# Optimization experiments

Measured on AMD Instinct MI355X. Metric: run time of the kernel, lower is better.

The kernel has to match this reference:

```python
import math
import jax, jax.numpy as jnp
import numpy as np

D_MODEL = 1024
N_HEADS = 16
HEAD_DIM = D_MODEL // N_HEADS
D_FF = 4096
LN_EPS = 1e-5


def _layer_norm(x, g, b):
    mu = jnp.mean(x, axis=-1, keepdims=True)
    var = jnp.var(x, axis=-1, keepdims=True)
    return (x - mu) * jax.lax.rsqrt(var + LN_EPS) * g + b


def setup_inputs() -> dict:
    key = jax.random.key(0)
    ks = jax.random.split(key, 8)
    s = 0.02
    d, dff = D_MODEL, D_FF
    return {
        "src": jax.random.normal(ks[0], (2, 2048, d), dtype=jnp.float32),
        "in_proj_w": jax.random.normal(ks[1], (3 * d, d), dtype=jnp.float32) * s,
        "in_proj_b": jnp.zeros((3 * d,), dtype=jnp.float32),
        "out_w": jax.random.normal(ks[2], (d, d), dtype=jnp.float32) * s,
        "out_b": jnp.zeros((d,), dtype=jnp.float32),
        "lin1_w": jax.random.normal(ks[3], (dff, d), dtype=jnp.float32) * s,
        "lin1_b": jnp.zeros((dff,), dtype=jnp.float32),
        "lin2_w": jax.random.normal(ks[4], (d, dff), dtype=jnp.float32) * s,
        "lin2_b": jnp.zeros((d,), dtype=jnp.float32),
        "ln1_g": jnp.ones((d,), dtype=jnp.float32),
        "ln1_b": jnp.zeros((d,), dtype=jnp.float32),
        "ln2_g": jnp.ones((d,), dtype=jnp.float32),
        "ln2_b": jnp.zeros((d,), dtype=jnp.float32),
    }


def reference(src, in_proj_w, in_proj_b, out_w, out_b, lin1_w, lin1_b,
              lin2_w, lin2_b, ln1_g, ln1_b, ln2_g, ln2_b):
    B, S, d = src.shape
    # QKV projections (in_proj_weight split at d, then kv split)
    q = src @ in_proj_w[:d].T + in_proj_b[:d]              # [B,S,d]
    kv = src @ in_proj_w[d:].T + in_proj_b[d:]             # [B,S,2d]
    q = q.reshape(B, S, N_HEADS, HEAD_DIM)
    kv = kv.reshape(B, S, 2, N_HEADS, HEAD_DIM)
    k, v = kv[:, :, 0], kv[:, :, 1]
    softmax_scale = 1.0 / math.sqrt(HEAD_DIM)
    scores = jnp.einsum('bthd,bshd->bhts', q, k) * softmax_scale  # [B,H,Sq,Skv]
    # 'distribute': softmax over the QUERY dimension (dim=-2)
    attention = jax.nn.softmax(scores, axis=-2)
    post = jnp.einsum('bhts,bshd->bthd', attention, v)     # [B,Sq,H,hd]
    # post-attention activation 'gelu' (torch exact gelu)
    post = jax.nn.gelu(post, approximate=False)
    # attention_scale == 'sqrt': divide by sqrt(kv_len)
    post = post / math.sqrt(S)
    attn_out = post.reshape(B, S, d) @ out_w.T + out_b
    # post-norm residual structure (pre_norm=False, dropout=0)
    x = _layer_norm(src + attn_out, ln1_g, ln1_b)
    ff = jax.nn.gelu(x @ lin1_w.T + lin1_b, approximate=False) @ lin2_w.T + lin2_b
    return _layer_norm(x + ff, ln2_g, ln2_b)
```

## Files before the change

### kernel.cpp

```cpp
#include <hip/hip_runtime.h>
#include <hip/hip_bf16.h>
#include <math.h>


using bf16x8 = __attribute__((ext_vector_type(8))) short;
using f32x4  = __attribute__((ext_vector_type(4))) float;

__device__ inline f32x4 mfma16(bf16x8 a, bf16x8 b, f32x4 c) {
    return __builtin_amdgcn_mfma_f32_16x16x32_bf16(a, b, c, 0, 0, 0);
}

__device__ inline ushort f2bf(float f) {
    union { float f; unsigned u; } x; x.f = f;
    unsigned r = x.u + 0x7fffu + ((x.u >> 16) & 1u);
    return (ushort)(r >> 16);
}

__device__ inline float bf2f(ushort u) {
    union { unsigned u; float f; } x; x.u = ((unsigned)u) << 16; return x.f;
}

__device__ inline unsigned pk2bf(float a, float b) {
    __hip_bfloat162 h = __float22bfloat162_rn(float2{a, b});
    union { __hip_bfloat162 h; unsigned u; } x; x.h = h;
    return x.u;
}

__device__ inline float gelu_fast(float v) {
    float u = v * (1.5957691216f + 0.0713548162f * v * v);
    float e = __expf(u);
    return v * (e / (e + 1.0f));
}

__device__ __forceinline__ void gl2lds16(const ushort* g, ushort* l) {
    __builtin_amdgcn_global_load_lds(
        (const __attribute__((address_space(1))) unsigned int*)g,
        (__attribute__((address_space(3))) unsigned int*)l,
        16, 0, 0);
}

__global__ __launch_bounds__(256) void cvt_all(const float4* __restrict__ s0,
                                               const float4* __restrict__ s1,
                                               const float4* __restrict__ s2,
                                               const float4* __restrict__ s3,
                                               const float4* __restrict__ s4,
                                               ushort4* __restrict__ out) {
    int i = blockIdx.x * 256 + threadIdx.x;
    const float4* p;
    int off;
    if (i < 1048576)      { p = s0; off = i; }
    else if (i < 1835008) { p = s1; off = i - 1048576; }
    else if (i < 2097152) { p = s2; off = i - 1835008; }
    else if (i < 3145728) { p = s3; off = i - 2097152; }
    else                  { p = s4; off = i - 3145728; }
    float4 v = p[off];
    ushort4 o;
    o.x = f2bf(v.x); o.y = f2bf(v.y); o.z = f2bf(v.z); o.w = f2bf(v.w);
    out[i] = o;
}

__global__ __launch_bounds__(256) void gemm_bt(
    const ushort* __restrict__ A, const ushort* __restrict__ Bw,
    const float* __restrict__ bias, int M, int N, int K, int kLen, int mode,
    ushort* __restrict__ ob0, ushort* __restrict__ ob1, ushort* __restrict__ ob2) {
    __shared__ ushort As[2][128 * 32];
    __shared__ ushort Bs[2][128 * 32];
    int tid = threadIdx.x, lane = tid & 63, w = tid >> 6;
    int wm = w >> 1, wn = w & 1;

    int Nx = gridDim.x, Ny = gridDim.y;
    int bx = blockIdx.x, by = blockIdx.y;
    if ((Ny & 7) == 0) {
        int i = bx + Nx * by;
        int c = i & 7, j = i >> 3;
        bx = j % Nx;
        by = c * (Ny >> 3) + j / Nx;
    }
    int bm = by * 128, bn = bx * 128;
    int kz = blockIdx.z;
    int q4 = lane >> 4, l15 = lane & 15;
    f32x4 acc[4][4] = {};

    int srow = w * 16 + (lane >> 2);
    int scg = lane & 3;
    const ushort* Ab = A + (size_t)bm * K + (size_t)kz * kLen;
    const ushort* Bb = Bw + (size_t)bn * K + (size_t)kz * kLen;
    const ushort* gA0 = Ab + (size_t)srow * K + scg * 8;
    const ushort* gA1 = Ab + (size_t)(64 + srow) * K + scg * 8;
    const ushort* gB0 = Bb + (size_t)srow * K + scg * 8;
    const ushort* gB1 = Bb + (size_t)(64 + srow) * K + scg * 8;
    ushort* lA00 = As[0] + w * 512;
    ushort* lA10 = As[0] + 2048 + w * 512;
    ushort* lB00 = Bs[0] + w * 512;
    ushort* lB10 = Bs[0] + 2048 + w * 512;
    ushort* lA01 = As[1] + w * 512;
    ushort* lA11 = As[1] + 2048 + w * 512;
    ushort* lB01 = Bs[1] + w * 512;
    ushort* lB11 = Bs[1] + 2048 + w * 512;

    const ushort* aB[2] = { &As[0][(wm * 64 + l15) * 32 + q4 * 8],
                            &As[1][(wm * 64 + l15) * 32 + q4 * 8] };
    const ushort* bB[2] = { &Bs[0][(wn * 64 + l15) * 32 + q4 * 8],
                            &Bs[1][(wn * 64 + l15) * 32 + q4 * 8] };

    for (int k0 = 0; k0 < kLen; k0 += 64) {
        __syncthreads();
        gl2lds16(gA0 + k0, lA00);
        gl2lds16(gA1 + k0, lA10);
        gl2lds16(gB0 + k0, lB00);
        gl2lds16(gB1 + k0, lB10);
        gl2lds16(gA0 + k0 + 32, lA01);
        gl2lds16(gA1 + k0 + 32, lA11);
        gl2lds16(gB0 + k0 + 32, lB01);
        gl2lds16(gB1 + k0 + 32, lB11);
        __syncthreads();
#pragma unroll
        for (int u = 0; u < 2; u++) {
            bf16x8 af[4], bfr[4];
#pragma unroll
            for (int mi = 0; mi < 4; mi++)
                af[mi] = *(const bf16x8*)(aB[u] + mi * 512);
#pragma unroll
            for (int ni = 0; ni < 4; ni++)
                bfr[ni] = *(const bf16x8*)(bB[u] + ni * 512);
#pragma unroll
            for (int mi = 0; mi < 4; mi++)
#pragma unroll
                for (int ni = 0; ni < 4; ni++)
                    acc[mi][ni] = mfma16(af[mi], bfr[ni], acc[mi][ni]);
        }
    }

    int r0 = bm + wm * 64, c0 = bn + wn * 64;
#pragma unroll
    for (int mi = 0; mi < 4; mi++) {
#pragma unroll
        for (int ni = 0; ni < 4; ni++) {
            int colg = c0 + ni * 16 + l15;
            float bv = (mode == 3) ? 0.f : bias[colg];
#pragma unroll
            for (int r = 0; r < 4; r++) {
                int rowg = r0 + mi * 16 + q4 * 4 + r;
                float v = acc[mi][ni][r] + bv;
                if (mode == 0) {
                    if (colg < 1024) {
                        ob0[(size_t)rowg * 1024 + colg] = f2bf(v);
                    } else if (colg < 2048) {
                        ob1[(size_t)rowg * 1024 + (colg - 1024)] = f2bf(v);
                    } else {
                        ob2[(size_t)rowg * 1024 + (colg - 2048)] = f2bf(v);
                    }
                } else if (mode == 2) {
                    ob0[(size_t)rowg * N + colg] = f2bf(gelu_fast(v));
                } else {
                    ob0[(size_t)kz * M * N + (size_t)rowg * N + colg] = f2bf(v);
                }
            }
        }
    }
}

__global__ __launch_bounds__(256) void attn_colsum_foldv(const ushort* __restrict__ qb,
                                                         const ushort* __restrict__ kb,
                                                         const ushort* __restrict__ vrow,
                                                         ushort* __restrict__ vt) {
    __shared__ ushort Qs[64 * 72];
    __shared__ float NinvS[128];
    int tid = threadIdx.x, lane = tid & 63, w = tid >> 6;
    int bh = blockIdx.x >> 4, sblk = blockIdx.x & 15;
    int b = bh >> 4, h = bh & 15;
    int q4 = lane >> 4, l15 = lane & 15;
    const ushort* qbase = qb + (size_t)(b * 2048) * 1024 + h * 64;
    const ushort* kbase = kb + (size_t)(b * 2048) * 1024 + h * 64;
    int s_base = sblk * 128 + w * 32;

    bf16x8 ka[2][2];
#pragma unroll
    for (int mi = 0; mi < 2; mi++) {
        const ushort* kp = kbase + (size_t)(s_base + mi * 16 + l15) * 1024 + q4 * 8;
        ka[mi][0] = *(const bf16x8*)(kp);
        ka[mi][1] = *(const bf16x8*)(kp + 32);
    }
    float acc[2][4] = {};

    int sr = tid >> 3;
    int sc = (tid & 7) * 8;
    for (int t0 = 0; t0 < 2048; t0 += 64) {
        uint4 g0 = *(const uint4*)(qbase + (size_t)(t0 + sr) * 1024 + sc);
        uint4 g1 = *(const uint4*)(qbase + (size_t)(t0 + 32 + sr) * 1024 + sc);
        __syncthreads();
        *(uint4*)&Qs[sr * 72 + sc] = g0;
        *(uint4*)&Qs[(32 + sr) * 72 + sc] = g1;
        __syncthreads();
#pragma unroll
        for (int tsub = 0; tsub < 4; tsub++) {
            bf16x8 bq0 = *(const bf16x8*)&Qs[(tsub * 16 + l15) * 72 + q4 * 8];
            bf16x8 bq1 = *(const bf16x8*)&Qs[(tsub * 16 + l15) * 72 + 32 + q4 * 8];
#pragma unroll
            for (int mi = 0; mi < 2; mi++) {
                f32x4 d = {0.f, 0.f, 0.f, 0.f};
                d = mfma16(ka[mi][0], bq0, d);
                d = mfma16(ka[mi][1], bq1, d);
#pragma unroll
                for (int r = 0; r < 4; r++)
                    acc[mi][r] += __expf(d[r] * 0.125f);
            }
        }
    }
#pragma unroll
    for (int mi = 0; mi < 2; mi++)
#pragma unroll
        for (int r = 0; r < 4; r++) {
            float v = acc[mi][r];
            v += __shfl_xor(v, 1); v += __shfl_xor(v, 2);
            v += __shfl_xor(v, 4); v += __shfl_xor(v, 8);
            if (l15 == 0)
                NinvS[w * 32 + mi * 16 + q4 * 4 + r] = 1.f / v;
        }

    int sl = tid >> 3, dh8 = (tid & 7) * 8;
#pragma unroll
    for (int batch = 0; batch < 2; batch++) {
        int bs = sblk * 128 + batch * 64;
        __syncthreads();
#pragma unroll
        for (int rep = 0; rep < 2; rep++) {
            int s = sl + rep * 32;
            float n = NinvS[batch * 64 + s];
            const ushort* p = vrow + (size_t)(b * 2048 + bs + s) * 1024 + h * 64 + dh8;
            ushort4 u0 = ((const ushort4*)p)[0];
            ushort4 u1 = ((const ushort4*)p)[1];
            ushort4 o0, o1;
            o0.x = f2bf(bf2f(u0.x) * n); o0.y = f2bf(bf2f(u0.y) * n);
            o0.z = f2bf(bf2f(u0.z) * n); o0.w = f2bf(bf2f(u0.w) * n);
            o1.x = f2bf(bf2f(u1.x) * n); o1.y = f2bf(bf2f(u1.y) * n);
            o1.z = f2bf(bf2f(u1.z) * n); o1.w = f2bf(bf2f(u1.w) * n);
            *(ushort4*)&Qs[s * 72 + dh8] = o0;
            *(ushort4*)&Qs[s * 72 + dh8 + 4] = o1;
        }
        __syncthreads();
        int dhl = tid >> 3, soff = (tid & 7) * 8;
#pragma unroll
        for (int rep = 0; rep < 2; rep++) {
            int d = dhl + rep * 32;
            ushort tmp[8];
#pragma unroll
            for (int j = 0; j < 8; j++) tmp[j] = Qs[(soff + j) * 72 + d];
            *(uint4*)(vt + ((size_t)bh * 64 + d) * 2048 + bs + soff) = *(uint4*)tmp;
        }
    }
}

__global__ __launch_bounds__(256) void attn_pv(const ushort* __restrict__ qb,
                                               const ushort* __restrict__ kb,
                                               const ushort* __restrict__ vt,
                                               ushort* __restrict__ post) {
    __shared__ ushort Ks[64 * 72];
    __shared__ ushort Vs[64 * 72];
    __shared__ ushort Ps[4][32 * 68];
    int tid = threadIdx.x, lane = tid & 63, w = tid >> 6;
    int bh = blockIdx.x >> 4, tblk = blockIdx.x & 15;
    int b = bh >> 4, h = bh & 15;
    int q4 = lane >> 4, l15 = lane & 15;
    const ushort* qbase = qb + (size_t)(b * 2048) * 1024 + h * 64;
    const ushort* kbase = kb + (size_t)(b * 2048) * 1024 + h * 64;
    const ushort* vtb = vt + (size_t)bh * 64 * 2048;
    int t_base = tblk * 128 + w * 32;

    bf16x8 aq[2][2];
#pragma unroll
    for (int mi = 0; mi < 2; mi++) {
        const ushort* qp = qbase + (size_t)(t_base + mi * 16 + l15) * 1024 + q4 * 8;
        aq[mi][0] = *(const bf16x8*)(qp);
        aq[mi][1] = *(const bf16x8*)(qp + 32);
    }
    f32x4 oacc[2][4] = {};
    ushort* myP = Ps[w];

    int sr = tid >> 3;
    int sc = (tid & 7) * 8;
    for (int s0 = 0; s0 < 2048; s0 += 64) {
        uint4 k0g = *(const uint4*)(kbase + (size_t)(s0 + sr) * 1024 + sc);
        uint4 k1g = *(const uint4*)(kbase + (size_t)(s0 + 32 + sr) * 1024 + sc);
        uint4 v0g = *(const uint4*)(vtb + (size_t)sr * 2048 + s0 + sc);
        uint4 v1g = *(const uint4*)(vtb + (size_t)(32 + sr) * 2048 + s0 + sc);
        __syncthreads();
        *(uint4*)&Ks[sr * 72 + sc] = k0g;
        *(uint4*)&Ks[(32 + sr) * 72 + sc] = k1g;
        *(uint4*)&Vs[sr * 72 + sc] = v0g;
        *(uint4*)&Vs[(32 + sr) * 72 + sc] = v1g;
        __syncthreads();
#pragma unroll
        for (int ssub = 0; ssub < 4; ssub++) {
            bf16x8 bk0 = *(const bf16x8*)&Ks[(ssub * 16 + l15) * 72 + q4 * 8];
            bf16x8 bk1 = *(const bf16x8*)&Ks[(ssub * 16 + l15) * 72 + 32 + q4 * 8];
#pragma unroll
            for (int mi = 0; mi < 2; mi++) {
                f32x4 d = {0.f, 0.f, 0.f, 0.f};
                d = mfma16(bk0, aq[mi][0], d);
                d = mfma16(bk1, aq[mi][1], d);
                float p0 = __expf(d[0] * 0.125f);
                float p1 = __expf(d[1] * 0.125f);
                float p2 = __expf(d[2] * 0.125f);
                float p3 = __expf(d[3] * 0.125f);
                uint2 uu;
                uu.x = pk2bf(p0, p1);
                uu.y = pk2bf(p2, p3);
                *(uint2*)&myP[(mi * 16 + l15) * 68 + ssub * 16 + q4 * 4] = uu;
            }
        }
        bf16x8 bv[4][2];
#pragma unroll
        for (int ni = 0; ni < 4; ni++) {
            bv[ni][0] = *(const bf16x8*)&Vs[(ni * 16 + l15) * 72 + q4 * 8];
            bv[ni][1] = *(const bf16x8*)&Vs[(ni * 16 + l15) * 72 + 32 + q4 * 8];
        }
#pragma unroll
        for (int mi = 0; mi < 2; mi++) {
            bf16x8 ap0 = *(const bf16x8*)&myP[(mi * 16 + l15) * 68 + q4 * 8];
            bf16x8 ap1 = *(const bf16x8*)&myP[(mi * 16 + l15) * 68 + 32 + q4 * 8];
#pragma unroll
            for (int ni = 0; ni < 4; ni++) {
                oacc[mi][ni] = mfma16(ap0, bv[ni][0], oacc[mi][ni]);
                oacc[mi][ni] = mfma16(ap1, bv[ni][1], oacc[mi][ni]);
            }
        }
    }
#pragma unroll
    for (int mi = 0; mi < 2; mi++)
#pragma unroll
        for (int ni = 0; ni < 4; ni++)
#pragma unroll
            for (int r = 0; r < 4; r++) {
                int t = t_base + mi * 16 + q4 * 4 + r;
                float g = gelu_fast(oacc[mi][ni][r]) * 0.022097086912079608f;
                post[(size_t)(b * 2048 + t) * 1024 + h * 64 + ni * 16 + l15] = f2bf(g);
            }
}

__global__ __launch_bounds__(256) void ln_comb4(const ushort* __restrict__ parts,
                                                const float* __restrict__ bias,
                                                const float* __restrict__ res,
                                                const float* __restrict__ gw,
                                                const float* __restrict__ bw,
                                                ushort* __restrict__ outb,
                                                float* __restrict__ outf) {
    const size_t PLANE = (size_t)4096 * 1024;
    int row = blockIdx.x, tid = threadIdx.x;
    int lane = tid & 63, wid = tid >> 6;
    size_t off = (size_t)row * 1024 + tid * 4;
    float4 r = *(const float4*)(res + off);
    float4 bb = *(const float4*)(bias + tid * 4);
    float4 v;
    v.x = r.x + bb.x; v.y = r.y + bb.y; v.z = r.z + bb.z; v.w = r.w + bb.w;
#pragma unroll
    for (int p = 0; p < 4; p++) {
        ushort4 u = *(const ushort4*)(parts + p * PLANE + off);
        v.x += bf2f(u.x); v.y += bf2f(u.y); v.z += bf2f(u.z); v.w += bf2f(u.w);
    }
    float s = v.x + v.y + v.z + v.w;
    float ss = v.x * v.x + v.y * v.y + v.z * v.z + v.w * v.w;
    for (int m = 1; m < 64; m <<= 1) { s += __shfl_xor(s, m); ss += __shfl_xor(ss, m); }
    __shared__ float red[8];
    if (lane == 0) { red[wid] = s; red[wid + 4] = ss; }
    __syncthreads();
    s = red[0] + red[1] + red[2] + red[3];
    ss = red[4] + red[5] + red[6] + red[7];
    float mu = s * (1.f / 1024.f);
    float var = ss * (1.f / 1024.f) - mu * mu;
    float inv = rsqrtf(var + 1e-5f);
    float4 gv = *(const float4*)(gw + tid * 4);
    float4 bv = *(const float4*)(bw + tid * 4);
    float o0 = (v.x - mu) * inv * gv.x + bv.x;
    float o1 = (v.y - mu) * inv * gv.y + bv.y;
    float o2 = (v.z - mu) * inv * gv.z + bv.z;
    float o3 = (v.w - mu) * inv * gv.w + bv.w;
    if (outf) {
        float4 o; o.x = o0; o.y = o1; o.z = o2; o.w = o3;
        *(float4*)(outf + off) = o;
    }
    if (outb) {
        ushort4 o; o.x = f2bf(o0); o.y = f2bf(o1); o.z = f2bf(o2); o.w = f2bf(o3);
        *(ushort4*)(outb + off) = o;
    }
}

extern "C" void kernel_launch(void* const* d_in, const int* in_sizes, int n_in,
                              void* d_out, int out_size, void* d_ws, size_t ws_size,
                              hipStream_t stream) {
    const float* src  = (const float*)d_in[0];
    const float* w_in = (const float*)d_in[1];
    const float* b_in = (const float*)d_in[2];
    const float* w_o  = (const float*)d_in[3];
    const float* b_o  = (const float*)d_in[4];
    const float* w1   = (const float*)d_in[5];
    const float* b1   = (const float*)d_in[6];
    const float* w2   = (const float*)d_in[7];
    const float* b2   = (const float*)d_in[8];
    const float* g1   = (const float*)d_in[9];
    const float* be1  = (const float*)d_in[10];
    const float* g2   = (const float*)d_in[11];
    const float* be2  = (const float*)d_in[12];
    float* out = (float*)d_out;

    const size_t M = 4096;
    char* wsp = (char*)d_ws;
    size_t off = 0;
    auto alloc = [&](size_t bytes) -> void* {
        void* p = wsp + off;
        off = (off + bytes + 255) & ~(size_t)255;
        return p;
    };
    ushort* src_bf  = (ushort*)alloc(M * 1024 * 2);
    ushort* win_bf  = (ushort*)alloc(3072 * 1024 * 2);
    ushort* wout_bf = (ushort*)alloc(1024 * 1024 * 2);
    ushort* w1_bf   = (ushort*)alloc(4096 * 1024 * 2);
    ushort* w2_bf   = (ushort*)alloc((size_t)1024 * 4096 * 2);
    ushort* q_bf    = (ushort*)alloc(M * 1024 * 2);
    ushort* k_bf    = (ushort*)alloc(M * 1024 * 2);
    ushort* vt_bf   = (ushort*)alloc(M * 1024 * 2);
    ushort* post_bf = (ushort*)alloc(M * 1024 * 2);
    ushort* part    = (ushort*)alloc(4 * M * 1024 * 2);
    ushort* x_bf    = (ushort*)alloc(M * 1024 * 2);
    float*  x_f32   = (float*)alloc(M * 1024 * 4);
    ushort* h1_bf   = (ushort*)alloc(M * 4096 * 2);
    ushort* v_row   = part;

    cvt_all<<<16384, 256, 0, stream>>>((const float4*)src, (const float4*)w_in,
                                       (const float4*)w_o, (const float4*)w1,
                                       (const float4*)w2, (ushort4*)src_bf);

    gemm_bt<<<dim3(24, 32, 1), 256, 0, stream>>>(src_bf, win_bf, b_in, 4096, 3072, 1024, 1024, 0,
                                                 q_bf, k_bf, v_row);

    attn_colsum_foldv<<<512, 256, 0, stream>>>(q_bf, k_bf, v_row, vt_bf);
    attn_pv<<<512, 256, 0, stream>>>(q_bf, k_bf, vt_bf, post_bf);

    gemm_bt<<<dim3(8, 32, 4), 256, 0, stream>>>(post_bf, wout_bf, b_o, 4096, 1024, 1024, 256, 3,
                                                part, nullptr, nullptr);
    ln_comb4<<<4096, 256, 0, stream>>>(part, b_o, src, g1, be1, x_bf, x_f32);

    gemm_bt<<<dim3(32, 32, 1), 256, 0, stream>>>(x_bf, w1_bf, b1, 4096, 4096, 1024, 1024, 2,
                                                 h1_bf, nullptr, nullptr);
    gemm_bt<<<dim3(8, 32, 4), 256, 0, stream>>>(h1_bf, w2_bf, b2, 4096, 1024, 4096, 1024, 3,
                                                part, nullptr, nullptr);
    ln_comb4<<<4096, 256, 0, stream>>>(part, b2, x_f32, g2, be2, nullptr, out);
}
```

Measured before the change: 482.2 us.

## Use direct global-to-LDS loads with XOR swizzle in attention; 2D XCD tile grouping

The attention kernels now load the Q, K and V tiles through direct global-to-LDS loads (gl2lds16) into unpadded 64-wide LDS rows with an XOR column swizzle. This replaces register staging and padding, which is meant to cut VGPR pressure, instruction count and bank conflicts. V fragments are now read from LDS inside the MFMA loop instead of being preloaded. Separately, the GEMM block remap takes a gx parameter so each of the 8 chiplet groups covers a 2D sub-grid of tiles rather than a row band, aiming for better L2 reuse.

```diff
diff --git a/kernel.cpp b/kernel.cpp
--- a/kernel.cpp
+++ b/kernel.cpp
@@ -61,7 +61,7 @@
 
 __global__ __launch_bounds__(256) void gemm_bt(
     const ushort* __restrict__ A, const ushort* __restrict__ Bw,
-    const float* __restrict__ bias, int M, int N, int K, int kLen, int mode,
+    const float* __restrict__ bias, int M, int N, int K, int kLen, int mode, int gx,
     ushort* __restrict__ ob0, ushort* __restrict__ ob1, ushort* __restrict__ ob2) {
     __shared__ ushort As[2][128 * 32];
     __shared__ ushort Bs[2][128 * 32];
@@ -70,11 +70,14 @@
 
     int Nx = gridDim.x, Ny = gridDim.y;
     int bx = blockIdx.x, by = blockIdx.y;
-    if ((Ny & 7) == 0) {
+    int gy = 8 / gx;
+    if ((Nx % gx) == 0 && (Ny % gy) == 0 && ((Nx * Ny) & 7) == 0) {
+        int Sx = Nx / gx, Sy = Ny / gy;
         int i = bx + Nx * by;
         int c = i & 7, j = i >> 3;
-        bx = j % Nx;
-        by = c * (Ny >> 3) + j / Nx;
+        int cx = c % gx, cy = c / gx;
+        bx = cx * Sx + j % Sx;
+        by = cy * Sy + (j / Sx) % Sy;
     }
     int bm = by * 128, bn = bx * 128;
     int kz = blockIdx.z;
@@ -183,19 +186,21 @@
     }
     float acc[2][4] = {};
 
-    int sr = tid >> 3;
-    int sc = (tid & 7) * 8;
+    int rl = lane >> 3;
+    int cswz = (((lane & 7) ^ rl) << 3);
+    int swf = l15 & 7;
+    int c0s = (q4 ^ swf) << 3;
+    int c1s = ((q4 + 4) ^ swf) << 3;
     for (int t0 = 0; t0 < 2048; t0 += 64) {
-        uint4 g0 = *(const uint4*)(qbase + (size_t)(t0 + sr) * 1024 + sc);
-        uint4 g1 = *(const uint4*)(qbase + (size_t)(t0 + 32 + sr) * 1024 + sc);
-        __syncthreads();
-        *(uint4*)&Qs[sr * 72 + sc] = g0;
-        *(uint4*)&Qs[(32 + sr) * 72 + sc] = g1;
+        __syncthreads();
+        gl2lds16(qbase + (size_t)(t0 + w * 16 + rl) * 1024 + cswz, Qs + (w * 16) * 64);
+        gl2lds16(qbase + (size_t)(t0 + w * 16 + 8 + rl) * 1024 + cswz, Qs + (w * 16 + 8) * 64);
         __syncthreads();
 #pragma unroll
         for (int tsub = 0; tsub < 4; tsub++) {
-            bf16x8 bq0 = *(const bf16x8*)&Qs[(tsub * 16 + l15) * 72 + q4 * 8];
-            bf16x8 bq1 = *(const bf16x8*)&Qs[(tsub * 16 + l15) * 72 + 32 + q4 * 8];
+            int rQ = (tsub * 16 + l15) * 64;
+            bf16x8 bq0 = *(const bf16x8*)&Qs[rQ + c0s];
+            bf16x8 bq1 = *(const bf16x8*)&Qs[rQ + c1s];
 #pragma unroll
             for (int mi = 0; mi < 2; mi++) {
                 f32x4 d = {0.f, 0.f, 0.f, 0.f};
@@ -255,8 +260,8 @@
                                                const ushort* __restrict__ kb,
                                                const ushort* __restrict__ vt,
                                                ushort* __restrict__ post) {
-    __shared__ ushort Ks[64 * 72];
-    __shared__ ushort Vs[64 * 72];
+    __shared__ ushort Ks[64 * 64];
+    __shared__ ushort Vs[64 * 64];
     __shared__ ushort Ps[4][32 * 68];
     int tid = threadIdx.x, lane = tid & 63, w = tid >> 6;
     int bh = blockIdx.x >> 4, tblk = blockIdx.x & 15;
@@ -277,23 +282,23 @@
     f32x4 oacc[2][4] = {};
     ushort* myP = Ps[w];
 
-    int sr = tid >> 3;
-    int sc = (tid & 7) * 8;
+    int rl = lane >> 3;
+    int cswz = (((lane & 7) ^ rl) << 3);
+    int swf = l15 & 7;
+    int c0s = (q4 ^ swf) << 3;
+    int c1s = ((q4 + 4) ^ swf) << 3;
     for (int s0 = 0; s0 < 2048; s0 += 64) {
-        uint4 k0g = *(const uint4*)(kbase + (size_t)(s0 + sr) * 1024 + sc);
-        uint4 k1g = *(const uint4*)(kbase + (size_t)(s0 + 32 + sr) * 1024 + sc);
-        uint4 v0g = *(const uint4*)(vtb + (size_t)sr * 2048 + s0 + sc);
-        uint4 v1g = *(const uint4*)(vtb + (size_t)(32 + sr) * 2048 + s0 + sc);
-        __syncthreads();
-        *(uint4*)&Ks[sr * 72 + sc] = k0g;
-        *(uint4*)&Ks[(32 + sr) * 72 + sc] = k1g;
-        *(uint4*)&Vs[sr * 72 + sc] = v0g;
-        *(uint4*)&Vs[(32 + sr) * 72 + sc] = v1g;
+        __syncthreads();
+        gl2lds16(kbase + (size_t)(s0 + w * 16 + rl) * 1024 + cswz, Ks + (w * 16) * 64);
+        gl2lds16(kbase + (size_t)(s0 + w * 16 + 8 + rl) * 1024 + cswz, Ks + (w * 16 + 8) * 64);
+        gl2lds16(vtb + (size_t)(w * 16 + rl) * 2048 + s0 + cswz, Vs + (w * 16) * 64);
+        gl2lds16(vtb + (size_t)(w * 16 + 8 + rl) * 2048 + s0 + cswz, Vs + (w * 16 + 8) * 64);
         __syncthreads();
 #pragma unroll
         for (int ssub = 0; ssub < 4; ssub++) {
-            bf16x8 bk0 = *(const bf16x8*)&Ks[(ssub * 16 + l15) * 72 + q4 * 8];
-            bf16x8 bk1 = *(const bf16x8*)&Ks[(ssub * 16 + l15) * 72 + 32 + q4 * 8];
+            int rA = (ssub * 16 + l15) * 64;
+            bf16x8 bk0 = *(const bf16x8*)&Ks[rA + c0s];
+            bf16x8 bk1 = *(const bf16x8*)&Ks[rA + c1s];
 #pragma unroll
             for (int mi = 0; mi < 2; mi++) {
                 f32x4 d = {0.f, 0.f, 0.f, 0.f};
@@ -309,20 +314,17 @@
                 *(uint2*)&myP[(mi * 16 + l15) * 68 + ssub * 16 + q4 * 4] = uu;
             }
         }
-        bf16x8 bv[4][2];
-#pragma unroll
-        for (int ni = 0; ni < 4; ni++) {
-            bv[ni][0] = *(const bf16x8*)&Vs[(ni * 16 + l15) * 72 + q4 * 8];
-            bv[ni][1] = *(const bf16x8*)&Vs[(ni * 16 + l15) * 72 + 32 + q4 * 8];
-        }
 #pragma unroll
         for (int mi = 0; mi < 2; mi++) {
             bf16x8 ap0 = *(const bf16x8*)&myP[(mi * 16 + l15) * 68 + q4 * 8];
             bf16x8 ap1 = *(const bf16x8*)&myP[(mi * 16 + l15) * 68 + 32 + q4 * 8];
 #pragma unroll
             for (int ni = 0; ni < 4; ni++) {
-                oacc[mi][ni] = mfma16(ap0, bv[ni][0], oacc[mi][ni]);
-                oacc[mi][ni] = mfma16(ap1, bv[ni][1], oacc[mi][ni]);
+                int rV = (ni * 16 + l15) * 64;
+                bf16x8 bv0 = *(const bf16x8*)&Vs[rV + c0s];
+                bf16x8 bv1 = *(const bf16x8*)&Vs[rV + c1s];
+                oacc[mi][ni] = mfma16(ap0, bv0, oacc[mi][ni]);
+                oacc[mi][ni] = mfma16(ap1, bv1, oacc[mi][ni]);
             }
         }
     }
@@ -430,19 +432,19 @@
                                        (const float4*)w_o, (const float4*)w1,
                                        (const float4*)w2, (ushort4*)src_bf);
 
-    gemm_bt<<<dim3(24, 32, 1), 256, 0, stream>>>(src_bf, win_bf, b_in, 4096, 3072, 1024, 1024, 0,
+    gemm_bt<<<dim3(24, 32, 1), 256, 0, stream>>>(src_bf, win_bf, b_in, 4096, 3072, 1024, 1024, 0, 2,
                                                  q_bf, k_bf, v_row);
 
     attn_colsum_foldv<<<512, 256, 0, stream>>>(q_bf, k_bf, v_row, vt_bf);
     attn_pv<<<512, 256, 0, stream>>>(q_bf, k_bf, vt_bf, post_bf);
 
-    gemm_bt<<<dim3(8, 32, 4), 256, 0, stream>>>(post_bf, wout_bf, b_o, 4096, 1024, 1024, 256, 3,
+    gemm_bt<<<dim3(8, 32, 4), 256, 0, stream>>>(post_bf, wout_bf, b_o, 4096, 1024, 1024, 256, 3, 1,
                                                 part, nullptr, nullptr);
     ln_comb4<<<4096, 256, 0, stream>>>(part, b_o, src, g1, be1, x_bf, x_f32);
 
-    gemm_bt<<<dim3(32, 32, 1), 256, 0, stream>>>(x_bf, w1_bf, b1, 4096, 4096, 1024, 1024, 2,
+    gemm_bt<<<dim3(32, 32, 1), 256, 0, stream>>>(x_bf, w1_bf, b1, 4096, 4096, 1024, 1024, 2, 2,
                                                  h1_bf, nullptr, nullptr);
-    gemm_bt<<<dim3(8, 32, 4), 256, 0, stream>>>(h1_bf, w2_bf, b2, 4096, 1024, 4096, 1024, 3,
+    gemm_bt<<<dim3(8, 32, 4), 256, 0, stream>>>(h1_bf, w2_bf, b2, 4096, 1024, 4096, 1024, 3, 1,
                                                 part, nullptr, nullptr);
     ln_comb4<<<4096, 256, 0, stream>>>(part, b2, x_f32, g2, be2, nullptr, out);
 }
```

Measured after the change: 469.9 us. 1.03x faster.
